# Kernel optimization log

Measured on AMD Instinct MI355X. Metric: run time of the kernel, lower is better.

The kernel has to match this reference:

```python
import jax, jax.numpy as jnp
import numpy as np

B, C, T, Fd = 4, 256, 64, 256
H = 8
HID = int(C * 2.0)
LN_EPS = 1e-5
L2_EPS = 1e-12


def _layernorm(x, g, b):
    mu = jnp.mean(x, axis=-1, keepdims=True)
    var = jnp.mean((x - mu) ** 2, axis=-1, keepdims=True)
    return (x - mu) * jax.lax.rsqrt(var + LN_EPS) * g + b


def _l2norm(x):
    n = jnp.sqrt(jnp.sum(x * x, axis=-1, keepdims=True))
    return x / jnp.maximum(n, L2_EPS)


def setup_inputs() -> dict:
    key = jax.random.key(0)
    ks = jax.random.split(key, 8)
    s = 0.02
    return {
        "x": jax.random.normal(ks[0], (B, C, T, Fd), dtype=jnp.float32),
        "norm1_g": jnp.ones((C,), jnp.float32),
        "norm1_b": jnp.zeros((C,), jnp.float32),
        "Wqkv": jax.random.normal(ks[1], (C, 3 * C), jnp.float32) * s,
        "dw_w": jax.random.normal(ks[2], (3 * C, 1, 3), jnp.float32) * s,  # depthwise conv1d kernel (O, I/g=1, K)
        "Wproj": jax.random.normal(ks[3], (C, C), jnp.float32) * s,
        "temperature": jnp.full((H, 1, 1), 0.5, jnp.float32),
        "norm2_g": jnp.ones((C,), jnp.float32),
        "norm2_b": jnp.zeros((C,), jnp.float32),
        "W1": jax.random.normal(ks[4], (C, HID), jnp.float32) * s,
        "b1": jnp.zeros((HID,), jnp.float32),
        "W2": jax.random.normal(ks[5], (HID, C), jnp.float32) * s,
        "b2": jnp.zeros((C,), jnp.float32),
    }


def reference(x, norm1_g, norm1_b, Wqkv, dw_w, Wproj, temperature,
              norm2_g, norm2_b, W1, b1, W2, b2):
    b, c, t, f = x.shape
    # axis='freq': (b c t f) -> ((b t) f c)
    xs = jnp.transpose(x, (0, 2, 3, 1)).reshape(b * t, f, c)

    xn = _layernorm(xs, norm1_g, norm1_b)
    qkv = xn @ Wqkv                                  # (bt, f, 3c)
    # depthwise conv1d along the sequence (freq) axis, kernel 3, pad 1
    qkv = jnp.transpose(qkv, (0, 2, 1))              # (bt, 3c, f)
    qkv = jax.lax.conv_general_dilated(
        qkv, dw_w, window_strides=(1,), padding=[(1, 1)],
        feature_group_count=3 * c,
        dimension_numbers=("NCH", "OIH", "NCH"))
    qkv = jnp.transpose(qkv, (0, 2, 1))              # (bt, f, 3c)

    q, k, v = jnp.split(qkv, 3, axis=-1)
    d = c // H
    def heads(z):  # (bt, s, c) -> (bt, h, s, d)
        return jnp.transpose(z.reshape(b * t, f, H, d), (0, 2, 1, 3))
    q, k, v = heads(q), heads(k), heads(v)

    q = _l2norm(q)
    k = _l2norm(k)
    attn = jnp.einsum("bhsd,bhtd->bhst", q, k) * temperature  # temp broadcasts (h,1,1)
    attn = jax.nn.softmax(attn, axis=-1)
    out = jnp.einsum("bhst,bhtd->bhsd", attn, v)
    out = jnp.transpose(out, (0, 2, 1, 3)).reshape(b * t, f, c)
    out = out @ Wproj
    out = out + xs

    h = _layernorm(out, norm2_g, norm2_b)
    h = jax.nn.gelu(h @ W1 + b1, approximate=False) @ W2 + b2
    out = out + h

    # ((b t) f c) -> (b c t f)
    out = out.reshape(b, t, f, c)
    return jnp.transpose(out, (0, 3, 1, 2))
```

## Files before the change

kernel.cpp:

```cpp
#include <hip/hip_runtime.h>
#include <math.h>

#define Bv 4
#define Cv 256
#define Tv 64
#define Fv 256
#define Hv 8
#define HIDv 512
#define Mv 65536
#define CTF (Cv * Tv * Fv)
#define TF (Tv * Fv)

typedef unsigned short u16;
typedef __attribute__((ext_vector_type(8))) short bfx8;
typedef __attribute__((ext_vector_type(4))) float f32x4;

__device__ __forceinline__ float bf2f(u16 u) {
  return __uint_as_float(((unsigned int)u) << 16);
}
__device__ __forceinline__ u16 f2bf(float f) {
  unsigned int x = __float_as_uint(f);
  unsigned int r = x + 0x7fffu + ((x >> 16) & 1u);
  return (u16)(r >> 16);
}

__launch_bounds__(256)
__global__ void transpose_w(const float* __restrict__ in, u16* __restrict__ out,
                            int K, int N) {
  __shared__ float t[32][33];
  const int n0 = blockIdx.x * 32, k0 = blockIdx.y * 32;
  const int c = threadIdx.x & 31, r = threadIdx.x >> 5;
#pragma unroll
  for (int i = 0; i < 4; ++i)
    t[r + 8 * i][c] = in[(size_t)(k0 + r + 8 * i) * N + n0 + c];
  __syncthreads();
#pragma unroll
  for (int i = 0; i < 4; ++i)
    out[(size_t)(n0 + r + 8 * i) * K + k0 + c] = f2bf(t[c][r + 8 * i]);
}

__launch_bounds__(256)
__global__ void ln1_kernel(const float* __restrict__ x, const float* __restrict__ g,
                           const float* __restrict__ bta, u16* __restrict__ xn) {
  __shared__ float tile[256][33];
  __shared__ float red1[8][32];
  __shared__ float red2[8][32];
  __shared__ float mu_s[32];
  __shared__ float rs_s[32];
  const int tid = threadIdx.x;
  const int blk = blockIdx.x;
  const int n = blk >> 3;
  const int f0 = (blk & 7) << 5;
  const int bb = n >> 6, tt = n & 63;
  const float* xb = x + (size_t)bb * CTF + (size_t)tt * Fv;
  const int fl = tid & 31, c0 = tid >> 5;
#pragma unroll
  for (int i = 0; i < 32; ++i) {
    int c = i * 8 + c0;
    tile[c][fl] = xb[(size_t)c * TF + f0 + fl];
  }
  __syncthreads();
  const int col = tid & 31, part = tid >> 5;
  float s = 0.f, s2 = 0.f;
#pragma unroll
  for (int i = 0; i < 32; ++i) {
    float v = tile[part * 32 + i][col];
    s += v; s2 += v * v;
  }
  red1[part][col] = s; red2[part][col] = s2;
  __syncthreads();
  if (tid < 32) {
    float S1 = 0.f, S2 = 0.f;
#pragma unroll
    for (int p = 0; p < 8; ++p) { S1 += red1[p][tid]; S2 += red2[p][tid]; }
    float m = S1 * (1.f / 256.f);
    float var = S2 * (1.f / 256.f) - m * m;
    mu_s[tid] = m;
    rs_s[tid] = rsqrtf(var + 1e-5f);
  }
  __syncthreads();
  const float gv = g[tid], bv = bta[tid];
  u16* ob = xn + ((size_t)n * 256 + f0) * 256 + tid;
#pragma unroll
  for (int fl2 = 0; fl2 < 32; ++fl2) {
    ob[(size_t)fl2 * 256] = f2bf((tile[tid][fl2] - mu_s[fl2]) * rs_s[fl2] * gv + bv);
  }
}

template <int K, int N, int EPI>
__launch_bounds__(256)
__global__ void gemm_mfma(const u16* __restrict__ A, const u16* __restrict__ Bt,
                          void* __restrict__ Cc, const float* __restrict__ aux0,
                          const u16* __restrict__ aux1) {
  constexpr int LDSTR = 88;
  __shared__ u16 As[128 * LDSTR];
  __shared__ u16 Bs[128 * LDSTR];
  const int tid = threadIdx.x;
  const int lane = tid & 63, wid = tid >> 6;
  const int m0 = blockIdx.y * 128, n0 = blockIdx.x * 128;
  const int wm = (wid & 1) * 64, wn = (wid >> 1) * 64;
  const int lm = lane & 15, quad = lane >> 4;

  const int srow = tid >> 3, sch = tid & 7;

  f32x4 acc[4][4] = {};
  for (int k0 = 0; k0 < K; k0 += 64) {
    bfx8 ar[4], br[4];
#pragma unroll
    for (int i = 0; i < 4; ++i) {
      const int row = srow + i * 32;
      ar[i] = *(const bfx8*)(A + (size_t)(m0 + row) * K + k0 + sch * 8);
      br[i] = *(const bfx8*)(Bt + (size_t)(n0 + row) * K + k0 + sch * 8);
    }
    __syncthreads();
#pragma unroll
    for (int i = 0; i < 4; ++i) {
      const int row = srow + i * 32;
      *(bfx8*)&As[row * LDSTR + sch * 8] = ar[i];
      *(bfx8*)&Bs[row * LDSTR + sch * 8] = br[i];
    }
    __syncthreads();
#pragma unroll
    for (int s = 0; s < 2; ++s) {
      bfx8 af[4], bf[4];
#pragma unroll
      for (int t = 0; t < 4; ++t) {
        af[t] = *(const bfx8*)&As[(wm + t * 16 + lm) * LDSTR + s * 32 + quad * 8];
        bf[t] = *(const bfx8*)&Bs[(wn + t * 16 + lm) * LDSTR + s * 32 + quad * 8];
      }
#pragma unroll
      for (int tm = 0; tm < 4; ++tm)
#pragma unroll
        for (int tn = 0; tn < 4; ++tn)
          acc[tm][tn] = __builtin_amdgcn_mfma_f32_16x16x32_bf16(af[tm], bf[tn], acc[tm][tn], 0, 0, 0);
    }
  }

  const int row_l = quad * 4;
  const int nn = m0 >> 8;
  const int bb = nn >> 6, tt = nn & 63;
  const int srow_base = (m0 & 255) + wm;
  float bcol[4];
  if constexpr (EPI == 2 || EPI == 3) {
#pragma unroll
    for (int tn = 0; tn < 4; ++tn) bcol[tn] = aux0[n0 + wn + tn * 16 + lm];
  }
#pragma unroll
  for (int tm = 0; tm < 4; ++tm) {
    const int grow0 = m0 + wm + tm * 16 + row_l;
    const int sr0 = srow_base + tm * 16 + row_l;
#pragma unroll
    for (int tn = 0; tn < 4; ++tn) {
      const int gcol = n0 + wn + tn * 16 + lm;
      if constexpr (EPI == 0) {
#pragma unroll
        for (int r = 0; r < 4; ++r)
          ((u16*)Cc)[(size_t)(grow0 + r) * N + gcol] = f2bf(acc[tm][tn][r]);
      } else if constexpr (EPI == 1) {
        const float4 xv = *(const float4*)(aux0 + (size_t)bb * CTF + (size_t)gcol * TF + tt * Fv + sr0);
        const float xr[4] = {xv.x, xv.y, xv.z, xv.w};
#pragma unroll
        for (int r = 0; r < 4; ++r)
          ((u16*)Cc)[(size_t)(grow0 + r) * N + gcol] = f2bf(acc[tm][tn][r] + xr[r]);
      } else if constexpr (EPI == 2) {
#pragma unroll
        for (int r = 0; r < 4; ++r) {
          float v = acc[tm][tn][r] + bcol[tn];
          float y = 0.79788456080286536f * (v + 0.044715f * v * v * v);
          float th = 1.f - 2.f / (__expf(2.f * y) + 1.f);
          ((u16*)Cc)[(size_t)(grow0 + r) * N + gcol] = f2bf(0.5f * v * (1.f + th));
        }
      } else {
        float4 o;
#pragma unroll
        for (int r = 0; r < 4; ++r) {
          float res = bf2f(aux1[(size_t)(grow0 + r) * 256 + gcol]);
          ((float*)&o)[r] = acc[tm][tn][r] + bcol[tn] + res;
        }
        *(float4*)((float*)Cc + (size_t)bb * CTF + (size_t)gcol * TF + tt * Fv + sr0) = o;
      }
    }
  }
}

__launch_bounds__(256)
__global__ void attn_kernel(const u16* __restrict__ qkv, const float* __restrict__ dw,
                            const float* __restrict__ temp, u16* __restrict__ attn_out) {
  __shared__ u16 Qs[256 * 40];
  __shared__ u16 Kc[64 * 40];
  __shared__ u16 Vtc[32 * 72];
  __shared__ u16 Pw[4 * 64 * 72];
  __shared__ float l_s[256];
  const int tid = threadIdx.x;
  const int lane = tid & 63, w = tid >> 6;
  const int l15 = lane & 15, quad = lane >> 4;
  const int n = blockIdx.x >> 3, h = blockIdx.x & 7;
  const int h32 = h * 32;
  const u16* base = qkv + (size_t)n * 256 * 768;
  const float th = temp[h];

  const int dg = tid & 3, d0 = dg * 8;
  const int rloc = tid >> 2;

  float wtsK[3][8], wtsV[3][8];
#pragma unroll
  for (int j = 0; j < 8; ++j) {
    const int chk = 256 + h32 + d0 + j;
    const int chv = 512 + h32 + d0 + j;
#pragma unroll
    for (int t = 0; t < 3; ++t) {
      wtsK[t][j] = dw[chk * 3 + t];
      wtsV[t][j] = dw[chv * 3 + t];
    }
  }

  {
    float wtsQ[3][8];
#pragma unroll
    for (int j = 0; j < 8; ++j)
#pragma unroll
      for (int t = 0; t < 3; ++t) wtsQ[t][j] = dw[(h32 + d0 + j) * 3 + t];
#pragma unroll
    for (int p = 0; p < 4; ++p) {
      const int row = p * 64 + rloc;
      const u16* src = base + (size_t)row * 768 + h32 + d0;
      float v[8];
      const bfx8 bmid = *(const bfx8*)src;
#pragma unroll
      for (int j = 0; j < 8; ++j) v[j] = wtsQ[1][j] * bf2f((u16)bmid[j]);
      if (row > 0) {
        const bfx8 bprv = *(const bfx8*)(src - 768);
#pragma unroll
        for (int j = 0; j < 8; ++j) v[j] += wtsQ[0][j] * bf2f((u16)bprv[j]);
      }
      if (row < 255) {
        const bfx8 bnxt = *(const bfx8*)(src + 768);
#pragma unroll
        for (int j = 0; j < 8; ++j) v[j] += wtsQ[2][j] * bf2f((u16)bnxt[j]);
      }
      float ssq = 0.f;
#pragma unroll
      for (int j = 0; j < 8; ++j) ssq += v[j] * v[j];
      ssq += __shfl_xor(ssq, 1);
      ssq += __shfl_xor(ssq, 2);
      const float inv = 1.f / fmaxf(sqrtf(ssq), 1e-12f);
      bfx8 qb;
#pragma unroll
      for (int j = 0; j < 8; ++j) qb[j] = (short)f2bf(v[j] * inv);
      *(bfx8*)&Qs[row * 40 + d0] = qb;
    }
  }
  __syncthreads();

  bfx8 bq[4];
#pragma unroll
  for (int ct = 0; ct < 4; ++ct)
    bq[ct] = *(const bfx8*)&Qs[(w * 64 + ct * 16 + l15) * 40 + quad * 8];

  u16* PwB = Pw + w * (64 * 72);
  const f32x4 zf = {0.f, 0.f, 0.f, 0.f};
  f32x4 acc[4][2] = {};
  float lsum[4] = {0.f, 0.f, 0.f, 0.f};

  for (int c = 0; c < 4; ++c) {
    {
      const int grow = c * 64 + rloc;
      const u16* srcK = base + (size_t)grow * 768 + 256 + h32 + d0;
      float v[8];
      const bfx8 bmid = *(const bfx8*)srcK;
#pragma unroll
      for (int j = 0; j < 8; ++j) v[j] = wtsK[1][j] * bf2f((u16)bmid[j]);
      if (grow > 0) {
        const bfx8 bprv = *(const bfx8*)(srcK - 768);
#pragma unroll
        for (int j = 0; j < 8; ++j) v[j] += wtsK[0][j] * bf2f((u16)bprv[j]);
      }
      if (grow < 255) {
        const bfx8 bnxt = *(const bfx8*)(srcK + 768);
#pragma unroll
        for (int j = 0; j < 8; ++j) v[j] += wtsK[2][j] * bf2f((u16)bnxt[j]);
      }
      float ssq = 0.f;
#pragma unroll
      for (int j = 0; j < 8; ++j) ssq += v[j] * v[j];
      ssq += __shfl_xor(ssq, 1);
      ssq += __shfl_xor(ssq, 2);
      const float inv = 1.f / fmaxf(sqrtf(ssq), 1e-12f);
      bfx8 kb;
#pragma unroll
      for (int j = 0; j < 8; ++j) kb[j] = (short)f2bf(v[j] * inv);
      *(bfx8*)&Kc[rloc * 40 + d0] = kb;

      const u16* srcV = base + (size_t)grow * 768 + 512 + h32 + d0;
      float vv[8];
      const bfx8 vmid = *(const bfx8*)srcV;
#pragma unroll
      for (int j = 0; j < 8; ++j) vv[j] = wtsV[1][j] * bf2f((u16)vmid[j]);
      if (grow > 0) {
        const bfx8 vprv = *(const bfx8*)(srcV - 768);
#pragma unroll
        for (int j = 0; j < 8; ++j) vv[j] += wtsV[0][j] * bf2f((u16)vprv[j]);
      }
      if (grow < 255) {
        const bfx8 vnxt = *(const bfx8*)(srcV + 768);
#pragma unroll
        for (int j = 0; j < 8; ++j) vv[j] += wtsV[2][j] * bf2f((u16)vnxt[j]);
      }
#pragma unroll
      for (int j = 0; j < 8; ++j) Vtc[(d0 + j) * 72 + rloc] = f2bf(vv[j]);
    }
    __syncthreads();

#pragma unroll
    for (int rt = 0; rt < 4; ++rt) {
      const bfx8 af = *(const bfx8*)&Kc[(rt * 16 + l15) * 40 + quad * 8];
#pragma unroll
      for (int ct = 0; ct < 4; ++ct) {
        f32x4 sc = __builtin_amdgcn_mfma_f32_16x16x32_bf16(af, bq[ct], zf, 0, 0, 0);
        float e0 = __expf(sc[0] * th);
        float e1 = __expf(sc[1] * th);
        float e2 = __expf(sc[2] * th);
        float e3 = __expf(sc[3] * th);
        lsum[ct] += (e0 + e1) + (e2 + e3);
        uint2 pk;
        pk.x = (unsigned int)f2bf(e0) | ((unsigned int)f2bf(e1) << 16);
        pk.y = (unsigned int)f2bf(e2) | ((unsigned int)f2bf(e3) << 16);
        *(uint2*)&PwB[(ct * 16 + l15) * 72 + rt * 16 + quad * 4] = pk;
      }
    }

#pragma unroll
    for (int ks = 0; ks < 2; ++ks) {
      const bfx8 bv0 = *(const bfx8*)&Vtc[l15 * 72 + ks * 32 + quad * 8];
      const bfx8 bv1 = *(const bfx8*)&Vtc[(16 + l15) * 72 + ks * 32 + quad * 8];
#pragma unroll
      for (int rt2 = 0; rt2 < 4; ++rt2) {
        const bfx8 ap = *(const bfx8*)&PwB[(rt2 * 16 + l15) * 72 + ks * 32 + quad * 8];
        acc[rt2][0] = __builtin_amdgcn_mfma_f32_16x16x32_bf16(ap, bv0, acc[rt2][0], 0, 0, 0);
        acc[rt2][1] = __builtin_amdgcn_mfma_f32_16x16x32_bf16(ap, bv1, acc[rt2][1], 0, 0, 0);
      }
    }
    __syncthreads();
  }

#pragma unroll
  for (int ct = 0; ct < 4; ++ct) {
    float L = lsum[ct];
    L += __shfl_xor(L, 16);
    L += __shfl_xor(L, 32);
    if (quad == 0) l_s[w * 64 + ct * 16 + l15] = L;
  }
  __syncthreads();

#pragma unroll
  for (int rt2 = 0; rt2 < 4; ++rt2) {
    const f32x4 l4 = *(const f32x4*)&l_s[w * 64 + rt2 * 16 + quad * 4];
    float rinv[4];
#pragma unroll
    for (int r = 0; r < 4; ++r) rinv[r] = 1.f / l4[r];
#pragma unroll
    for (int ct2 = 0; ct2 < 2; ++ct2) {
#pragma unroll
      for (int r = 0; r < 4; ++r) {
        const int qrow = w * 64 + rt2 * 16 + quad * 4 + r;
        attn_out[((size_t)n * 256 + qrow) * 256 + h32 + ct2 * 16 + l15] =
            f2bf(acc[rt2][ct2][r] * rinv[r]);
      }
    }
  }
}

__launch_bounds__(256)
__global__ void ln2_kernel(const u16* __restrict__ in, const float* __restrict__ g,
                           const float* __restrict__ bta, u16* __restrict__ out) {
  const int lane = threadIdx.x & 63;
  const size_t row = (size_t)blockIdx.x * 4 + (threadIdx.x >> 6);
  const ushort4 u = ((const ushort4*)(in + row * 256))[lane];
  const float vx = bf2f(u.x), vy = bf2f(u.y), vz = bf2f(u.z), vw = bf2f(u.w);
  float s = vx + vy + vz + vw;
  float s2 = vx * vx + vy * vy + vz * vz + vw * vw;
#pragma unroll
  for (int m = 32; m >= 1; m >>= 1) {
    s += __shfl_xor(s, m, 64);
    s2 += __shfl_xor(s2, m, 64);
  }
  const float mu = s * (1.f / 256.f);
  const float rs = rsqrtf(s2 * (1.f / 256.f) - mu * mu + 1e-5f);
  const float4 gv = ((const float4*)g)[lane];
  const float4 bv = ((const float4*)bta)[lane];
  ushort4 o;
  o.x = f2bf((vx - mu) * rs * gv.x + bv.x);
  o.y = f2bf((vy - mu) * rs * gv.y + bv.y);
  o.z = f2bf((vz - mu) * rs * gv.z + bv.z);
  o.w = f2bf((vw - mu) * rs * gv.w + bv.w);
  ((ushort4*)(out + row * 256))[lane] = o;
}

extern "C" void kernel_launch(void* const* d_in, const int* in_sizes, int n_in,
                              void* d_out, int out_size, void* d_ws, size_t ws_size,
                              hipStream_t stream) {
  const float* x     = (const float*)d_in[0];
  const float* n1g   = (const float*)d_in[1];
  const float* n1b   = (const float*)d_in[2];
  const float* Wqkv  = (const float*)d_in[3];
  const float* dw    = (const float*)d_in[4];
  const float* Wproj = (const float*)d_in[5];
  const float* temp  = (const float*)d_in[6];
  const float* n2g   = (const float*)d_in[7];
  const float* n2b   = (const float*)d_in[8];
  const float* W1    = (const float*)d_in[9];
  const float* b1    = (const float*)d_in[10];
  const float* W2    = (const float*)d_in[11];
  const float* b2    = (const float*)d_in[12];

  char* ws = (char*)d_ws;
  u16* xn       = (u16*)(ws);
  u16* qkv      = (u16*)(ws + (32ull << 20));
  u16* attn_out = xn;
  u16* out1     = (u16*)(ws + (32ull << 20));
  u16* xn2      = xn;
  u16* h1       = (u16*)(ws + (64ull << 20));
  u16* w2t      = xn;

  char* ob = (char*)d_out;
  u16* wqkvt  = (u16*)(ob);
  u16* wprojt = (u16*)(ob + (1ull << 20));
  u16* w1t    = (u16*)(ob + 1572864ull);

  transpose_w<<<dim3(24, 8), 256, 0, stream>>>(Wqkv, wqkvt, 256, 768);
  transpose_w<<<dim3(8, 8), 256, 0, stream>>>(Wproj, wprojt, 256, 256);
  transpose_w<<<dim3(16, 8), 256, 0, stream>>>(W1, w1t, 256, 512);

  ln1_kernel<<<2048, 256, 0, stream>>>(x, n1g, n1b, xn);
  gemm_mfma<256, 768, 0><<<dim3(6, 512), 256, 0, stream>>>(xn, wqkvt, qkv, nullptr, nullptr);
  attn_kernel<<<2048, 256, 0, stream>>>(qkv, dw, temp, attn_out);
  gemm_mfma<256, 256, 1><<<dim3(2, 512), 256, 0, stream>>>(attn_out, wprojt, out1, x, nullptr);
  ln2_kernel<<<16384, 256, 0, stream>>>(out1, n2g, n2b, xn2);
  gemm_mfma<256, 512, 2><<<dim3(4, 512), 256, 0, stream>>>(xn2, W1 ? w1t : w1t, h1, b1, nullptr);
  transpose_w<<<dim3(8, 16), 256, 0, stream>>>(W2, w2t, 512, 256);
  gemm_mfma<512, 256, 3><<<dim3(2, 512), 256, 0, stream>>>(h1, w2t, d_out, b2, out1);
}
```

Before: 413.6 us.

## Restructure attention kernel: 512 threads, double-buffered K/V, register-resident P via permlane

The attention kernel now runs with 8 waves per block, each owning 32 query rows held in registers, so the shared Q buffer goes away. K and V chunks are double-buffered in shared memory, and the next chunk's global loads are issued before the current chunk's MFMAs, with one barrier per chunk. Softmax probabilities are packed with v_cvt_pk_bf16 and rearranged into MFMA operand layout with permlane swaps instead of a round trip through LDS. V is produced by warp-specialised threads using a sliding window and a swizzled transposed store, and exp uses exp2 with a prescaled temperature. This adds more register pressure and relies on gfx950-specific permlane and convert instructions.

```diff
diff --git a/kernel.cpp b/kernel.cpp
--- a/kernel.cpp
+++ b/kernel.cpp
@@ -22,6 +22,11 @@
   unsigned int x = __float_as_uint(f);
   unsigned int r = x + 0x7fffu + ((x >> 16) & 1u);
   return (u16)(r >> 16);
+}
+__device__ __forceinline__ unsigned int cvtpk(float a, float b) {
+  unsigned int r;
+  asm("v_cvt_pk_bf16_f32 %0, %1, %2" : "=v"(r) : "v"(a), "v"(b));
+  return r;
 }
 
 __launch_bounds__(256)
@@ -183,13 +188,11 @@
   }
 }
 
-__launch_bounds__(256)
+__launch_bounds__(512, 4)
 __global__ void attn_kernel(const u16* __restrict__ qkv, const float* __restrict__ dw,
                             const float* __restrict__ temp, u16* __restrict__ attn_out) {
-  __shared__ u16 Qs[256 * 40];
-  __shared__ u16 Kc[64 * 40];
-  __shared__ u16 Vtc[32 * 72];
-  __shared__ u16 Pw[4 * 64 * 72];
+  __shared__ u16 Kc[2][64 * 40];
+  __shared__ u16 Vt[2][32 * 72];
   __shared__ float l_s[256];
   const int tid = threadIdx.x;
   const int lane = tid & 63, w = tid >> 6;
@@ -197,176 +200,183 @@
   const int n = blockIdx.x >> 3, h = blockIdx.x & 7;
   const int h32 = h * 32;
   const u16* base = qkv + (size_t)n * 256 * 768;
-  const float th = temp[h];
-
-  const int dg = tid & 3, d0 = dg * 8;
-  const int rloc = tid >> 2;
-
-  float wtsK[3][8], wtsV[3][8];
-#pragma unroll
-  for (int j = 0; j < 8; ++j) {
-    const int chk = 256 + h32 + d0 + j;
-    const int chv = 512 + h32 + d0 + j;
-#pragma unroll
-    for (int t = 0; t < 3; ++t) {
-      wtsK[t][j] = dw[chk * 3 + t];
-      wtsV[t][j] = dw[chv * 3 + t];
-    }
-  }
-
+  const float th2 = temp[h] * 1.44269504089f;
+
+  bfx8 bq[2];
   {
-    float wtsQ[3][8];
+    const int d0q = quad * 8;
+    float wq[3][8];
 #pragma unroll
     for (int j = 0; j < 8; ++j)
 #pragma unroll
-      for (int t = 0; t < 3; ++t) wtsQ[t][j] = dw[(h32 + d0 + j) * 3 + t];
-#pragma unroll
-    for (int p = 0; p < 4; ++p) {
-      const int row = p * 64 + rloc;
-      const u16* src = base + (size_t)row * 768 + h32 + d0;
+      for (int t = 0; t < 3; ++t) wq[t][j] = dw[(h32 + d0q + j) * 3 + t];
+#pragma unroll
+    for (int ct = 0; ct < 2; ++ct) {
+      const int row = w * 32 + ct * 16 + l15;
+      const u16* src = base + (size_t)row * 768 + h32 + d0q;
       float v[8];
-      const bfx8 bmid = *(const bfx8*)src;
-#pragma unroll
-      for (int j = 0; j < 8; ++j) v[j] = wtsQ[1][j] * bf2f((u16)bmid[j]);
+      const bfx8 bm = *(const bfx8*)src;
+#pragma unroll
+      for (int j = 0; j < 8; ++j) v[j] = wq[1][j] * bf2f((u16)bm[j]);
       if (row > 0) {
-        const bfx8 bprv = *(const bfx8*)(src - 768);
-#pragma unroll
-        for (int j = 0; j < 8; ++j) v[j] += wtsQ[0][j] * bf2f((u16)bprv[j]);
+        const bfx8 bp = *(const bfx8*)(src - 768);
+#pragma unroll
+        for (int j = 0; j < 8; ++j) v[j] += wq[0][j] * bf2f((u16)bp[j]);
       }
       if (row < 255) {
-        const bfx8 bnxt = *(const bfx8*)(src + 768);
-#pragma unroll
-        for (int j = 0; j < 8; ++j) v[j] += wtsQ[2][j] * bf2f((u16)bnxt[j]);
-      }
+        const bfx8 bn = *(const bfx8*)(src + 768);
+#pragma unroll
+        for (int j = 0; j < 8; ++j) v[j] += wq[2][j] * bf2f((u16)bn[j]);
+      }
+      float ssq = 0.f;
+#pragma unroll
+      for (int j = 0; j < 8; ++j) ssq += v[j] * v[j];
+      ssq += __shfl_xor(ssq, 16);
+      ssq += __shfl_xor(ssq, 32);
+      const float inv = 1.f / fmaxf(sqrtf(ssq), 1e-12f);
+      union { unsigned int u[4]; bfx8 b; } qb;
+#pragma unroll
+      for (int m = 0; m < 4; ++m) qb.u[m] = cvtpk(v[2 * m] * inv, v[2 * m + 1] * inv);
+      bq[ct] = qb.b;
+    }
+  }
+
+  const bool isK = tid < 256;
+  const int sV = tid & 255;
+  const int krow = sV >> 2, kd0 = (sV & 3) * 8;
+  const int vd = sV & 31, vko = sV >> 5;
+  float wu[24];
+  if (isK) {
+#pragma unroll
+    for (int j = 0; j < 8; ++j)
+#pragma unroll
+      for (int t = 0; t < 3; ++t) wu[t * 8 + j] = dw[(256 + h32 + kd0 + j) * 3 + t];
+  } else {
+#pragma unroll
+    for (int t = 0; t < 3; ++t) wu[t] = dw[(512 + h32 + vd) * 3 + t];
+  }
+
+  bfx8 km = {}, kp = {}, kn = {};
+  u16 xs[10];
+
+  auto stage_load = [&](int c) {
+    if (isK) {
+      const int gr = c * 64 + krow;
+      const u16* src = base + (size_t)gr * 768 + 256 + h32 + kd0;
+      km = *(const bfx8*)src;
+      kp = (gr > 0) ? *(const bfx8*)(src - 768) : bfx8{};
+      kn = (gr < 255) ? *(const bfx8*)(src + 768) : bfx8{};
+    } else {
+      const int g0 = c * 64 + vko * 8;
+      const u16* src = base + (size_t)g0 * 768 + 512 + h32 + vd;
+#pragma unroll
+      for (int k = 0; k < 10; ++k) {
+        const int gr = g0 + k - 1;
+        xs[k] = (gr >= 0 && gr < 256) ? src[(ptrdiff_t)(k - 1) * 768] : (u16)0;
+      }
+    }
+  };
+  auto stage_finish = [&](int b) {
+    if (isK) {
+      float v[8];
+#pragma unroll
+      for (int j = 0; j < 8; ++j)
+        v[j] = wu[8 + j] * bf2f((u16)km[j]) + wu[j] * bf2f((u16)kp[j]) +
+               wu[16 + j] * bf2f((u16)kn[j]);
       float ssq = 0.f;
 #pragma unroll
       for (int j = 0; j < 8; ++j) ssq += v[j] * v[j];
       ssq += __shfl_xor(ssq, 1);
       ssq += __shfl_xor(ssq, 2);
       const float inv = 1.f / fmaxf(sqrtf(ssq), 1e-12f);
-      bfx8 qb;
-#pragma unroll
-      for (int j = 0; j < 8; ++j) qb[j] = (short)f2bf(v[j] * inv);
-      *(bfx8*)&Qs[row * 40 + d0] = qb;
-    }
-  }
+      union { unsigned int u[4]; bfx8 b; } kb;
+#pragma unroll
+      for (int m = 0; m < 4; ++m) kb.u[m] = cvtpk(v[2 * m] * inv, v[2 * m + 1] * inv);
+      *(bfx8*)&Kc[b][krow * 40 + kd0] = kb.b;
+    } else {
+      float x[10];
+#pragma unroll
+      for (int k = 0; k < 10; ++k) x[k] = bf2f(xs[k]);
+      union { unsigned int u[4]; bfx8 b; } ob;
+#pragma unroll
+      for (int m = 0; m < 4; ++m) {
+        float a0 = wu[0] * x[2 * m] + wu[1] * x[2 * m + 1] + wu[2] * x[2 * m + 2];
+        float a1 = wu[0] * x[2 * m + 1] + wu[1] * x[2 * m + 2] + wu[2] * x[2 * m + 3];
+        ob.u[m] = cvtpk(a0, a1);
+      }
+      const int po = vko ^ ((vd >> 3) & 3);
+      *(bfx8*)&Vt[b][vd * 72 + po * 8] = ob.b;
+    }
+  };
+
+  f32x4 acc[2][2] = {};
+  float lsum[2] = {0.f, 0.f};
+  const f32x4 zf = {0.f, 0.f, 0.f, 0.f};
+  const int fo = (l15 >> 3) & 1;
+
+  stage_load(0);
+  stage_finish(0);
   __syncthreads();
 
-  bfx8 bq[4];
-#pragma unroll
-  for (int ct = 0; ct < 4; ++ct)
-    bq[ct] = *(const bfx8*)&Qs[(w * 64 + ct * 16 + l15) * 40 + quad * 8];
-
-  u16* PwB = Pw + w * (64 * 72);
-  const f32x4 zf = {0.f, 0.f, 0.f, 0.f};
-  f32x4 acc[4][2] = {};
-  float lsum[4] = {0.f, 0.f, 0.f, 0.f};
-
   for (int c = 0; c < 4; ++c) {
-    {
-      const int grow = c * 64 + rloc;
-      const u16* srcK = base + (size_t)grow * 768 + 256 + h32 + d0;
-      float v[8];
-      const bfx8 bmid = *(const bfx8*)srcK;
-#pragma unroll
-      for (int j = 0; j < 8; ++j) v[j] = wtsK[1][j] * bf2f((u16)bmid[j]);
-      if (grow > 0) {
-        const bfx8 bprv = *(const bfx8*)(srcK - 768);
-#pragma unroll
-        for (int j = 0; j < 8; ++j) v[j] += wtsK[0][j] * bf2f((u16)bprv[j]);
-      }
-      if (grow < 255) {
-        const bfx8 bnxt = *(const bfx8*)(srcK + 768);
-#pragma unroll
-        for (int j = 0; j < 8; ++j) v[j] += wtsK[2][j] * bf2f((u16)bnxt[j]);
-      }
-      float ssq = 0.f;
-#pragma unroll
-      for (int j = 0; j < 8; ++j) ssq += v[j] * v[j];
-      ssq += __shfl_xor(ssq, 1);
-      ssq += __shfl_xor(ssq, 2);
-      const float inv = 1.f / fmaxf(sqrtf(ssq), 1e-12f);
-      bfx8 kb;
-#pragma unroll
-      for (int j = 0; j < 8; ++j) kb[j] = (short)f2bf(v[j] * inv);
-      *(bfx8*)&Kc[rloc * 40 + d0] = kb;
-
-      const u16* srcV = base + (size_t)grow * 768 + 512 + h32 + d0;
-      float vv[8];
-      const bfx8 vmid = *(const bfx8*)srcV;
-#pragma unroll
-      for (int j = 0; j < 8; ++j) vv[j] = wtsV[1][j] * bf2f((u16)vmid[j]);
-      if (grow > 0) {
-        const bfx8 vprv = *(const bfx8*)(srcV - 768);
-#pragma unroll
-        for (int j = 0; j < 8; ++j) vv[j] += wtsV[0][j] * bf2f((u16)vprv[j]);
-      }
-      if (grow < 255) {
-        const bfx8 vnxt = *(const bfx8*)(srcV + 768);
-#pragma unroll
-        for (int j = 0; j < 8; ++j) vv[j] += wtsV[2][j] * bf2f((u16)vnxt[j]);
-      }
-#pragma unroll
-      for (int j = 0; j < 8; ++j) Vtc[(d0 + j) * 72 + rloc] = f2bf(vv[j]);
-    }
+    const int b = c & 1;
+    if (c < 3) stage_load(c + 1);
+
+    bfx8 af[4];
+#pragma unroll
+    for (int rt = 0; rt < 4; ++rt)
+      af[rt] = *(const bfx8*)&Kc[b][(rt * 16 + l15) * 40 + quad * 8];
+#pragma unroll
+    for (int ct = 0; ct < 2; ++ct) {
+      unsigned int pu[4], pv[4];
+#pragma unroll
+      for (int rt = 0; rt < 4; ++rt) {
+        f32x4 sc = __builtin_amdgcn_mfma_f32_16x16x32_bf16(af[rt], bq[ct], zf, 0, 0, 0);
+        float e0 = exp2f(sc[0] * th2), e1 = exp2f(sc[1] * th2);
+        float e2 = exp2f(sc[2] * th2), e3 = exp2f(sc[3] * th2);
+        lsum[ct] += (e0 + e1) + (e2 + e3);
+        pu[rt] = cvtpk(e0, e1);
+        pv[rt] = cvtpk(e2, e3);
+      }
+#pragma unroll
+      for (int ks = 0; ks < 2; ++ks) {
+        auto su = __builtin_amdgcn_permlane32_swap(pu[2 * ks], pu[2 * ks + 1], false, false);
+        auto tu = __builtin_amdgcn_permlane16_swap(su[0], su[1], false, false);
+        auto sv = __builtin_amdgcn_permlane32_swap(pv[2 * ks], pv[2 * ks + 1], false, false);
+        auto tv = __builtin_amdgcn_permlane16_swap(sv[0], sv[1], false, false);
+        union { unsigned int u[4]; bfx8 b; } ap;
+        ap.u[0] = tu[0]; ap.u[1] = tv[0]; ap.u[2] = tu[1]; ap.u[3] = tv[1];
+        const bfx8 bv0 = *(const bfx8*)&Vt[b][l15 * 72 + (ks * 4 + (quad ^ fo)) * 8];
+        const bfx8 bv1 = *(const bfx8*)&Vt[b][(16 + l15) * 72 + (ks * 4 + (quad ^ (2 | fo))) * 8];
+        acc[ct][0] = __builtin_amdgcn_mfma_f32_16x16x32_bf16(ap.b, bv0, acc[ct][0], 0, 0, 0);
+        acc[ct][1] = __builtin_amdgcn_mfma_f32_16x16x32_bf16(ap.b, bv1, acc[ct][1], 0, 0, 0);
+      }
+    }
+    if (c < 3) stage_finish(b ^ 1);
     __syncthreads();
-
-#pragma unroll
-    for (int rt = 0; rt < 4; ++rt) {
-      const bfx8 af = *(const bfx8*)&Kc[(rt * 16 + l15) * 40 + quad * 8];
-#pragma unroll
-      for (int ct = 0; ct < 4; ++ct) {
-        f32x4 sc = __builtin_amdgcn_mfma_f32_16x16x32_bf16(af, bq[ct], zf, 0, 0, 0);
-        float e0 = __expf(sc[0] * th);
-        float e1 = __expf(sc[1] * th);
-        float e2 = __expf(sc[2] * th);
-        float e3 = __expf(sc[3] * th);
-        lsum[ct] += (e0 + e1) + (e2 + e3);
-        uint2 pk;
-        pk.x = (unsigned int)f2bf(e0) | ((unsigned int)f2bf(e1) << 16);
-        pk.y = (unsigned int)f2bf(e2) | ((unsigned int)f2bf(e3) << 16);
-        *(uint2*)&PwB[(ct * 16 + l15) * 72 + rt * 16 + quad * 4] = pk;
-      }
-    }
-
-#pragma unroll
-    for (int ks = 0; ks < 2; ++ks) {
-      const bfx8 bv0 = *(const bfx8*)&Vtc[l15 * 72 + ks * 32 + quad * 8];
-      const bfx8 bv1 = *(const bfx8*)&Vtc[(16 + l15) * 72 + ks * 32 + quad * 8];
-#pragma unroll
-      for (int rt2 = 0; rt2 < 4; ++rt2) {
-        const bfx8 ap = *(const bfx8*)&PwB[(rt2 * 16 + l15) * 72 + ks * 32 + quad * 8];
-        acc[rt2][0] = __builtin_amdgcn_mfma_f32_16x16x32_bf16(ap, bv0, acc[rt2][0], 0, 0, 0);
-        acc[rt2][1] = __builtin_amdgcn_mfma_f32_16x16x32_bf16(ap, bv1, acc[rt2][1], 0, 0, 0);
-      }
-    }
-    __syncthreads();
-  }
-
-#pragma unroll
-  for (int ct = 0; ct < 4; ++ct) {
+  }
+
+#pragma unroll
+  for (int ct = 0; ct < 2; ++ct) {
     float L = lsum[ct];
     L += __shfl_xor(L, 16);
     L += __shfl_xor(L, 32);
-    if (quad == 0) l_s[w * 64 + ct * 16 + l15] = L;
-  }
-  __syncthreads();
-
-#pragma unroll
-  for (int rt2 = 0; rt2 < 4; ++rt2) {
-    const f32x4 l4 = *(const f32x4*)&l_s[w * 64 + rt2 * 16 + quad * 4];
+    if (quad == 0) l_s[w * 32 + ct * 16 + l15] = L;
+  }
+#pragma unroll
+  for (int ct = 0; ct < 2; ++ct) {
+    const f32x4 l4 = *(const f32x4*)&l_s[w * 32 + ct * 16 + quad * 4];
     float rinv[4];
 #pragma unroll
     for (int r = 0; r < 4; ++r) rinv[r] = 1.f / l4[r];
 #pragma unroll
-    for (int ct2 = 0; ct2 < 2; ++ct2) {
+    for (int dh = 0; dh < 2; ++dh)
 #pragma unroll
       for (int r = 0; r < 4; ++r) {
-        const int qrow = w * 64 + rt2 * 16 + quad * 4 + r;
-        attn_out[((size_t)n * 256 + qrow) * 256 + h32 + ct2 * 16 + l15] =
-            f2bf(acc[rt2][ct2][r] * rinv[r]);
-      }
-    }
+        const int qrow = w * 32 + ct * 16 + quad * 4 + r;
+        attn_out[((size_t)n * 256 + qrow) * 256 + h32 + dh * 16 + l15] =
+            f2bf(acc[ct][dh][r] * rinv[r]);
+      }
   }
 }
 
@@ -433,7 +443,7 @@
 
   ln1_kernel<<<2048, 256, 0, stream>>>(x, n1g, n1b, xn);
   gemm_mfma<256, 768, 0><<<dim3(6, 512), 256, 0, stream>>>(xn, wqkvt, qkv, nullptr, nullptr);
-  attn_kernel<<<2048, 256, 0, stream>>>(qkv, dw, temp, attn_out);
+  attn_kernel<<<2048, 512, 0, stream>>>(qkv, dw, temp, attn_out);
   gemm_mfma<256, 256, 1><<<dim3(2, 512), 256, 0, stream>>>(attn_out, wprojt, out1, x, nullptr);
   ln2_kernel<<<16384, 256, 0, stream>>>(out1, n2g, n2b, xn2);
   gemm_mfma<256, 512, 2><<<dim3(4, 512), 256, 0, stream>>>(xn2, W1 ? w1t : w1t, h1, b1, nullptr);
```

After: 519.4 us. +25.6%, slower.
